# Optimization experiments

Hardware: AMD Instinct MI355X
Metric: run time of the kernel (lower is better)

The kernel has to match this reference:

```python
import jax, jax.numpy as jnp
import numpy as np

N = 100000
IN_CH, HID_CH, OUT_CH = 128, 128, 64
E = 1600000


def gcn_layer(x, W, b, src, dst, num_nodes):
    """PyG GCNConv: add self-loops, symmetric deg^-1/2 normalization,
    x' = D^-1/2 (A+I) D^-1/2 (x W) + b."""
    # degrees including self-loops (deg = 1 + in-degree with unit edge weights)
    ones = jnp.ones(dst.shape[0], dtype=x.dtype)
    deg = jnp.ones(num_nodes, dtype=x.dtype).at[dst].add(ones)
    dinv = jax.lax.rsqrt(deg)
    h = x @ W  # [N, out_dim] -- transform before propagate (PyG order)
    # neighbor messages
    norm = dinv[src] * dinv[dst]                      # [E]
    msg = h[src] * norm[:, None]                      # [E, out_dim] (traffic-bound)
    agg = jax.ops.segment_sum(msg, dst, num_segments=num_nodes)
    # self-loop contribution: norm_ii = dinv[i]^2
    agg = agg + h * (dinv * dinv)[:, None]
    return agg + b


def setup_inputs() -> dict:
    key = jax.random.key(0)
    ks = jax.random.split(key, 7)
    x = jax.random.normal(ks[0], (N, IN_CH), dtype=jnp.float32)
    edge_index = jax.random.randint(ks[1], (2, E), 0, N, dtype=jnp.int64)
    # Glorot-style init like PyG GCNConv
    W1 = jax.random.normal(ks[2], (IN_CH, HID_CH), dtype=jnp.float32) * (1.0 / np.sqrt(IN_CH))
    b1 = jnp.zeros((HID_CH,), dtype=jnp.float32)
    W2 = jax.random.normal(ks[3], (HID_CH, OUT_CH), dtype=jnp.float32) * (1.0 / np.sqrt(HID_CH))
    b2 = jnp.zeros((OUT_CH,), dtype=jnp.float32)
    return {"x": x, "edge_index": edge_index, "W1": W1, "b1": b1, "W2": W2, "b2": b2}


def reference(x, edge_index, W1, b1, W2, b2):
    src, dst = edge_index[0], edge_index[1]
    h = gcn_layer(x, W1, b1, src, dst, N)
    h = jax.nn.relu(h)  # dropout is identity in eval mode
    out = gcn_layer(h, W2, b2, src, dst, N)
    return out
```

## Files before the change

### kernel.cpp

```cpp
#include <hip/hip_runtime.h>
#include <hip/hip_fp16.h>

#define NNODES 100000
#define NEDGES 1600000
#define IN_C   128
#define HID_C  128
#define OUT_C  64

#define CAP     64
#define OVF_MAX 4096

#define BUCKET_SHIFT 7
#define BUCKET_NODES 128
#define NB ((NNODES + BUCKET_NODES - 1) / BUCKET_NODES)
#define BCAP 3072
#define BCNT_STRIDE 16
#define EB 4096
#define NBLK_A ((NEDGES + EB - 1) / EB)
#define GB ((NNODES + 63) / 64)

typedef __attribute__((ext_vector_type(8))) _Float16 half8;
typedef __attribute__((ext_vector_type(4))) _Float16 half4;
typedef __attribute__((ext_vector_type(4))) float floatx4;

__device__ __forceinline__ long long load_idx(const void* p, long long i, int is64) {
  return is64 ? ((const long long*)p)[i] : (long long)((const int*)p)[i];
}

__global__ void prep_kernel(const void* eidx, int* flag, int* bcnt,
                            int* ovf_cnt, int* ovfA_cnt,
                            const float* __restrict__ W1,
                            const float* __restrict__ W2,
                            _Float16* __restrict__ Wt1,
                            _Float16* __restrict__ Wt2) {
  int i = blockIdx.x * 256 + threadIdx.x;
  if (i < NB * BCNT_STRIDE) bcnt[i] = 0;
  if (i == 0) { *ovf_cnt = 0; *ovfA_cnt = 0; }
  if (blockIdx.x == 0 && threadIdx.x < 64) {
    const unsigned* w = (const unsigned*)eidx;
    unsigned v = w[2 * threadIdx.x + 1];
    unsigned long long bad = __ballot(v != 0u);
    if (threadIdx.x == 0) *flag = (bad == 0ull) ? 1 : 0;
  }
  const int stride = gridDim.x * 256;
  for (int t = i; t < IN_C * HID_C; t += stride) {
    int n = t >> 7, k = t & 127;
    Wt1[t] = (_Float16)W1[k * HID_C + n];
  }
  for (int t = i; t < HID_C * OUT_C; t += stride) {
    int n = t >> 7, k = t & 127;
    Wt2[t] = (_Float16)W2[k * OUT_C + n];
  }
}

__global__ __launch_bounds__(512) void binA_kernel(const void* __restrict__ eidx,
                                                   const int* __restrict__ flag,
                                                   int* __restrict__ bcnt,
                                                   unsigned* __restrict__ buf,
                                                   int* __restrict__ ovfA_cnt,
                                                   int2* __restrict__ ovfA) {
  __shared__ unsigned se[EB];
  __shared__ unsigned short be[EB];
  __shared__ int hist[NB];
  __shared__ int base[NB];
  __shared__ int ofs[NB];
  const int tid = threadIdx.x;
  const int e0 = blockIdx.x * EB;
  const int e1 = min(e0 + EB, NEDGES);
  const int m = e1 - e0;
  const int is64 = *flag;

  for (int b = tid; b < NB; b += 512) { hist[b] = 0; ofs[b] = 0; }
  __syncthreads();

  for (int k = tid; k < m; k += 512) {
    int e = e0 + k;
    int s = (int)load_idx(eidx, e, is64);
    int d = (int)load_idx(eidx, (long long)NEDGES + e, is64);
    int b = d >> BUCKET_SHIFT;
    se[k] = (unsigned)s | ((unsigned)(d & (BUCKET_NODES - 1)) << 17);
    be[k] = (unsigned short)b;
    atomicAdd(&hist[b], 1);
  }
  __syncthreads();

  int rot = (blockIdx.x * 131) % NB;
  for (int idx = tid; idx < NB; idx += 512) {
    int b = idx + rot;
    if (b >= NB) b -= NB;
    int h = hist[b];
    if (h > 0) base[b] = atomicAdd(&bcnt[b * BCNT_STRIDE], h);
  }
  __syncthreads();

  for (int k = tid; k < m; k += 512) {
    unsigned u = se[k];
    int b = be[k];
    int ko = atomicAdd(&ofs[b], 1);
    int slot = base[b] + ko;
    if (slot < BCAP) {
      buf[(size_t)b * BCAP + slot] = u;
    } else {
      int p = atomicAdd(ovfA_cnt, 1);
      if (p < OVF_MAX)
        ovfA[p] = make_int2((int)(u & 0x1FFFFu),
                            (b << BUCKET_SHIFT) | (int)(u >> 17));
    }
  }
}

__global__ __launch_bounds__(512) void binB_kernel(const int* __restrict__ bcnt,
                                                   const unsigned* __restrict__ buf,
                                                   const int* __restrict__ ovfA_cnt,
                                                   const int2* __restrict__ ovfA,
                                                   int* __restrict__ cnt,
                                                   float* __restrict__ dinv,
                                                   int* __restrict__ pad_csr,
                                                   int* __restrict__ ovf_cnt,
                                                   int2* __restrict__ ovf) {
  __shared__ int pad[BUCKET_NODES * CAP];
  __shared__ int lcnt[BUCKET_NODES];
  const int b = blockIdx.x;
  const int tid = threadIdx.x;
  const int node0 = b << BUCKET_SHIFT;

  if (tid < BUCKET_NODES) lcnt[tid] = 0;
  __syncthreads();

  const int n = min(bcnt[b * BCNT_STRIDE], BCAP);
  for (int k = tid; k < n; k += 512) {
    unsigned u = buf[(size_t)b * BCAP + k];
    int s = (int)(u & 0x1FFFFu);
    int dl = (int)(u >> 17);
    int slot = atomicAdd(&lcnt[dl], 1);
    if (slot < CAP) {
      pad[dl * CAP + slot] = s;
    } else {
      int p = atomicAdd(ovf_cnt, 1);
      if (p < OVF_MAX) ovf[p] = make_int2(s, node0 + dl);
    }
  }
  int na = min(*ovfA_cnt, OVF_MAX);
  for (int t = tid; t < na; t += 512) {
    int2 p = ovfA[t];
    if ((p.y >> BUCKET_SHIFT) == b) {
      int dl = p.y & (BUCKET_NODES - 1);
      int slot = atomicAdd(&lcnt[dl], 1);
      if (slot < CAP) {
        pad[dl * CAP + slot] = p.x;
      } else {
        int q = atomicAdd(ovf_cnt, 1);
        if (q < OVF_MAX) ovf[q] = make_int2(p.x, p.y);
      }
    }
  }
  __syncthreads();

  constexpr int I4PN = CAP / 4;
  for (int q = tid; q < BUCKET_NODES * I4PN; q += 512) {
    int dl = q / I4PN;
    int gn = node0 + dl;
    if (gn < NNODES) {
      int c = (q % I4PN) * 4;
      *(int4*)&pad_csr[(size_t)gn * CAP + c] = *(const int4*)&pad[dl * CAP + c];
    }
  }
  if (tid < BUCKET_NODES && node0 + tid < NNODES) {
    int c = lcnt[tid];
    cnt[node0 + tid] = c;
    dinv[node0 + tid] = rsqrtf((float)(c + 1));
  }
}

__global__ __launch_bounds__(256) void gemm1_kernel(const float* __restrict__ x,
                                                    const _Float16* __restrict__ Wt1,
                                                    const float* __restrict__ dinv,
                                                    _Float16* __restrict__ h1s) {
  constexpr int K = IN_C, N = HID_C, KP = K + 8;
  __shared__ alignas(16) _Float16 Alds[64 * KP];
  __shared__ alignas(16) _Float16 Wlds[N * KP];
  const int tid = threadIdx.x;
  const int row0 = blockIdx.x * 64;

  for (int idx = tid; idx < N * (K / 8); idx += 256) {
    int n = idx >> 4, k16 = idx & 15;
    *(int4*)&Wlds[n * KP + k16 * 8] = *(const int4*)&Wt1[n * K + k16 * 8];
  }
  constexpr int F4PR = K / 4;
  for (int idx = tid; idx < 64 * F4PR; idx += 256) {
    int lr = idx >> 5;
    int c4 = (idx & 31) * 4;
    int gr = row0 + lr;
    if (gr > NNODES - 1) gr = NNODES - 1;
    float4 v = *(const float4*)&x[(size_t)gr * K + c4];
    half4 h = {(_Float16)v.x, (_Float16)v.y, (_Float16)v.z, (_Float16)v.w};
    *(half4*)&Alds[lr * KP + c4] = h;
  }
  __syncthreads();

  const int w = tid >> 6;
  const int lane = tid & 63;
  const int g = lane >> 4;
  const int mi = lane & 15;
  constexpr int NT = N / 16;
  floatx4 acc[NT];
#pragma unroll
  for (int t = 0; t < NT; ++t) acc[t] = (floatx4){0.f, 0.f, 0.f, 0.f};
  const _Float16* arow = &Alds[(w * 16 + mi) * KP];
#pragma unroll
  for (int ks = 0; ks < K / 32; ++ks) {
    half8 a = *(const half8*)(arow + ks * 32 + g * 8);
#pragma unroll
    for (int t = 0; t < NT; ++t) {
      half8 b = *(const half8*)&Wlds[(t * 16 + mi) * KP + ks * 32 + g * 8];
      acc[t] = __builtin_amdgcn_mfma_f32_16x16x32_f16(a, b, acc[t], 0, 0, 0);
    }
  }
#pragma unroll
  for (int r = 0; r < 4; ++r) {
    int grow = row0 + w * 16 + 4 * g + r;
    if (grow < NNODES) {
      float s = dinv[grow];
      _Float16* orow = h1s + (size_t)grow * N + mi;
#pragma unroll
      for (int t = 0; t < NT; ++t) orow[t * 16] = (_Float16)(acc[t][r] * s);
    }
  }
}

__global__ __launch_bounds__(256) void gemm2_kernel(const _Float16* __restrict__ hid,
                                                    const _Float16* __restrict__ Wt2,
                                                    const float* __restrict__ dinv,
                                                    _Float16* __restrict__ h2s) {
  constexpr int K = HID_C, N = OUT_C, KP = K + 8;
  __shared__ alignas(16) _Float16 Alds[64 * KP];
  __shared__ alignas(16) _Float16 Wlds[N * KP];
  const int tid = threadIdx.x;
  const int row0 = blockIdx.x * 64;

  for (int idx = tid; idx < N * (K / 8); idx += 256) {
    int n = idx >> 4, k16 = idx & 15;
    *(int4*)&Wlds[n * KP + k16 * 8] = *(const int4*)&Wt2[n * K + k16 * 8];
  }
  for (int idx = tid; idx < 64 * (K / 8); idx += 256) {
    int lr = idx >> 4, k16 = idx & 15;
    int gr = row0 + lr;
    if (gr > NNODES - 1) gr = NNODES - 1;
    *(int4*)&Alds[lr * KP + k16 * 8] =
        *(const int4*)&hid[(size_t)gr * K + k16 * 8];
  }
  __syncthreads();

  const int w = tid >> 6;
  const int lane = tid & 63;
  const int g = lane >> 4;
  const int mi = lane & 15;
  constexpr int NT = N / 16;
  floatx4 acc[NT];
#pragma unroll
  for (int t = 0; t < NT; ++t) acc[t] = (floatx4){0.f, 0.f, 0.f, 0.f};
  const _Float16* arow = &Alds[(w * 16 + mi) * KP];
#pragma unroll
  for (int ks = 0; ks < K / 32; ++ks) {
    half8 a = *(const half8*)(arow + ks * 32 + g * 8);
#pragma unroll
    for (int t = 0; t < NT; ++t) {
      half8 b = *(const half8*)&Wlds[(t * 16 + mi) * KP + ks * 32 + g * 8];
      acc[t] = __builtin_amdgcn_mfma_f32_16x16x32_f16(a, b, acc[t], 0, 0, 0);
    }
  }
#pragma unroll
  for (int r = 0; r < 4; ++r) {
    int grow = row0 + w * 16 + 4 * g + r;
    if (grow < NNODES) {
      float s = dinv[grow];
      _Float16* orow = h2s + (size_t)grow * N + mi;
#pragma unroll
      for (int t = 0; t < NT; ++t) orow[t * 16] = (_Float16)(acc[t][r] * s);
    }
  }
}

struct F8 {
  float x0, x1, x2, x3, x4, x5, x6, x7;
};

__device__ __forceinline__ void add_h8(F8& a, const __half* p) {
  int4 r = *(const int4*)p;
  const __half2* h = (const __half2*)&r;
  float2 f0 = __half22float2(h[0]);
  float2 f1 = __half22float2(h[1]);
  float2 f2 = __half22float2(h[2]);
  float2 f3 = __half22float2(h[3]);
  a.x0 += f0.x; a.x1 += f0.y; a.x2 += f1.x; a.x3 += f1.y;
  a.x4 += f2.x; a.x5 += f2.y; a.x6 += f3.x; a.x7 += f3.y;
}

template <int C, bool RELU, bool OUT16>
__global__ __launch_bounds__(256) void gather_kernel(const int* __restrict__ cnt,
                                                     const int* __restrict__ pad_csr,
                                                     const float* __restrict__ dinv,
                                                     const __half* __restrict__ Hs,
                                                     const float* __restrict__ bias,
                                                     const int* __restrict__ ovf_cnt,
                                                     const int2* __restrict__ ovf,
                                                     void* __restrict__ OutPtr) {
  constexpr int TPN = C / 16;
  int gid = blockIdx.x * 256 + threadIdx.x;
  int i = gid / TPN;
  int c16 = (gid % TPN) * 16;
  if (i >= NNODES) return;

  const float di = dinv[i];
  const int deg = cnt[i];
  const int beg = i * CAP;
  const int end = beg + min(deg, CAP);
  const int* __restrict__ lst = pad_csr;
  const __half* __restrict__ Hb = Hs + c16;

  F8 a0l = {}, a0h = {}, a1l = {}, a1h = {};
  {
    const __half* p = Hb + (size_t)i * C;
    add_h8(a0l, p);
    add_h8(a0h, p + 8);
  }

  int j = beg;
  for (; j + 8 <= end; j += 8) {
    int4 sa = *(const int4*)&lst[j];
    int4 sb = *(const int4*)&lst[j + 4];
    const __half* p0 = Hb + (size_t)sa.x * C;
    const __half* p1 = Hb + (size_t)sa.y * C;
    const __half* p2 = Hb + (size_t)sa.z * C;
    const __half* p3 = Hb + (size_t)sa.w * C;
    add_h8(a0l, p0); add_h8(a0h, p0 + 8);
    add_h8(a1l, p1); add_h8(a1h, p1 + 8);
    add_h8(a0l, p2); add_h8(a0h, p2 + 8);
    add_h8(a1l, p3); add_h8(a1h, p3 + 8);
    const __half* p4 = Hb + (size_t)sb.x * C;
    const __half* p5 = Hb + (size_t)sb.y * C;
    const __half* p6 = Hb + (size_t)sb.z * C;
    const __half* p7 = Hb + (size_t)sb.w * C;
    add_h8(a0l, p4); add_h8(a0h, p4 + 8);
    add_h8(a1l, p5); add_h8(a1h, p5 + 8);
    add_h8(a0l, p6); add_h8(a0h, p6 + 8);
    add_h8(a1l, p7); add_h8(a1h, p7 + 8);
  }
  for (; j + 2 <= end; j += 2) {
    const __half* p0 = Hb + (size_t)lst[j] * C;
    const __half* p1 = Hb + (size_t)lst[j + 1] * C;
    add_h8(a0l, p0); add_h8(a0h, p0 + 8);
    add_h8(a1l, p1); add_h8(a1h, p1 + 8);
  }
  if (j < end) {
    const __half* p0 = Hb + (size_t)lst[j] * C;
    add_h8(a0l, p0); add_h8(a0h, p0 + 8);
  }

  if (deg > CAP) {
    int n = min(*ovf_cnt, OVF_MAX);
    for (int t = 0; t < n; ++t) {
      int2 p = ovf[t];
      if (p.y == i) {
        const __half* q = Hb + (size_t)p.x * C;
        add_h8(a0l, q); add_h8(a0h, q + 8);
      }
    }
  }

  float s0 = a0l.x0 + a1l.x0, s1 = a0l.x1 + a1l.x1;
  float s2 = a0l.x2 + a1l.x2, s3 = a0l.x3 + a1l.x3;
  float s4 = a0l.x4 + a1l.x4, s5 = a0l.x5 + a1l.x5;
  float s6 = a0l.x6 + a1l.x6, s7 = a0l.x7 + a1l.x7;
  float s8 = a0h.x0 + a1h.x0, s9 = a0h.x1 + a1h.x1;
  float s10 = a0h.x2 + a1h.x2, s11 = a0h.x3 + a1h.x3;
  float s12 = a0h.x4 + a1h.x4, s13 = a0h.x5 + a1h.x5;
  float s14 = a0h.x6 + a1h.x6, s15 = a0h.x7 + a1h.x7;

  float4 b0 = *(const float4*)&bias[c16];
  float4 b1 = *(const float4*)&bias[c16 + 4];
  float4 b2 = *(const float4*)&bias[c16 + 8];
  float4 b3 = *(const float4*)&bias[c16 + 12];
  float o0 = fmaf(s0, di, b0.x),  o1 = fmaf(s1, di, b0.y);
  float o2 = fmaf(s2, di, b0.z),  o3 = fmaf(s3, di, b0.w);
  float o4 = fmaf(s4, di, b1.x),  o5 = fmaf(s5, di, b1.y);
  float o6 = fmaf(s6, di, b1.z),  o7 = fmaf(s7, di, b1.w);
  float o8 = fmaf(s8, di, b2.x),  o9 = fmaf(s9, di, b2.y);
  float o10 = fmaf(s10, di, b2.z), o11 = fmaf(s11, di, b2.w);
  float o12 = fmaf(s12, di, b3.x), o13 = fmaf(s13, di, b3.y);
  float o14 = fmaf(s14, di, b3.z), o15 = fmaf(s15, di, b3.w);
  if (RELU) {
    o0 = o0 > 0.f ? o0 : 0.f;   o1 = o1 > 0.f ? o1 : 0.f;
    o2 = o2 > 0.f ? o2 : 0.f;   o3 = o3 > 0.f ? o3 : 0.f;
    o4 = o4 > 0.f ? o4 : 0.f;   o5 = o5 > 0.f ? o5 : 0.f;
    o6 = o6 > 0.f ? o6 : 0.f;   o7 = o7 > 0.f ? o7 : 0.f;
    o8 = o8 > 0.f ? o8 : 0.f;   o9 = o9 > 0.f ? o9 : 0.f;
    o10 = o10 > 0.f ? o10 : 0.f; o11 = o11 > 0.f ? o11 : 0.f;
    o12 = o12 > 0.f ? o12 : 0.f; o13 = o13 > 0.f ? o13 : 0.f;
    o14 = o14 > 0.f ? o14 : 0.f; o15 = o15 > 0.f ? o15 : 0.f;
  }
  if (OUT16) {
    _Float16* Out = (_Float16*)OutPtr + (size_t)i * C + c16;
    half8 hv0 = {(_Float16)o0, (_Float16)o1, (_Float16)o2, (_Float16)o3,
                 (_Float16)o4, (_Float16)o5, (_Float16)o6, (_Float16)o7};
    half8 hv1 = {(_Float16)o8, (_Float16)o9, (_Float16)o10, (_Float16)o11,
                 (_Float16)o12, (_Float16)o13, (_Float16)o14, (_Float16)o15};
    *(half8*)Out = hv0;
    *(half8*)(Out + 8) = hv1;
  } else {
    float* Out = (float*)OutPtr + (size_t)i * C + c16;
    *(float4*)Out = make_float4(o0, o1, o2, o3);
    *(float4*)(Out + 4) = make_float4(o4, o5, o6, o7);
    *(float4*)(Out + 8) = make_float4(o8, o9, o10, o11);
    *(float4*)(Out + 12) = make_float4(o12, o13, o14, o15);
  }
}

extern "C" void kernel_launch(void* const* d_in, const int* in_sizes, int n_in,
                              void* d_out, int out_size, void* d_ws, size_t ws_size,
                              hipStream_t stream) {
  const float* x = (const float*)d_in[0];
  const void* eidx = d_in[1];
  const float* W1 = (const float*)d_in[2];
  const float* b1 = (const float*)d_in[3];
  const float* W2 = (const float*)d_in[4];
  const float* b2 = (const float*)d_in[5];
  float* out = (float*)d_out;
  char* ws = (char*)d_ws;

  int*      flag     = (int*)(ws + 0);
  int*      ovf_cnt  = (int*)(ws + 512);
  int*      ovfA_cnt = (int*)(ws + 1024);
  int*      bcnt     = (int*)(ws + 1536);
  int*      cnt      = (int*)(ws + 52224);
  float*    dinv     = (float*)(ws + 452608);
  int2*     ovf      = (int2*)(ws + 852992);
  int2*     ovfA     = (int2*)(ws + 885760);
  _Float16* Wt1      = (_Float16*)(ws + 918528);
  _Float16* Wt2      = (_Float16*)(ws + 951296);
  unsigned* buf      = (unsigned*)(ws + 968192);
  int*      pad_csr  = (int*)(ws + 10577920);
  _Float16* h1s      = (_Float16*)(ws + 36178432);
  _Float16* hidden   = (_Float16*)(ws + 61778944);
  _Float16* h2s      = h1s;

  prep_kernel<<<(NB * BCNT_STRIDE + 255) / 256, 256, 0, stream>>>(
      eidx, flag, bcnt, ovf_cnt, ovfA_cnt, W1, W2, Wt1, Wt2);
  binA_kernel<<<NBLK_A, 512, 0, stream>>>(eidx, flag, bcnt, buf, ovfA_cnt, ovfA);
  binB_kernel<<<NB, 512, 0, stream>>>(bcnt, buf, ovfA_cnt, ovfA, cnt, dinv,
                                      pad_csr, ovf_cnt, ovf);
  gemm1_kernel<<<GB, 256, 0, stream>>>(x, Wt1, dinv, h1s);
  gather_kernel<HID_C, true, true>
      <<<(NNODES * (HID_C / 16) + 255) / 256, 256, 0, stream>>>(
          cnt, pad_csr, dinv, (const __half*)h1s, b1, ovf_cnt, ovf, hidden);
  gemm2_kernel<<<GB, 256, 0, stream>>>(hidden, Wt2, dinv, h2s);
  gather_kernel<OUT_C, false, false>
      <<<(NNODES * (OUT_C / 16) + 255) / 256, 256, 0, stream>>>(
          cnt, pad_csr, dinv, (const __half*)h2s, b2, ovf_cnt, ovf, out);
}
```

Measured before the change: 270.4 us.

## Fuse graph-build kernels into one cooperative kernel and halve padded CSR capacity

Merges the prep, bin-A and bin-B kernels into a single cooperative kernel that uses grid-wide syncs between phases, removing two kernel launches and their gaps. It also reduces the per-node padded neighbour capacity from 64 to 32, which halves pad_csr writes and gather index reads. The catch is that more nodes exceed the capacity and go to the overflow path, where the overflow list is capped at 4096 entries. Cooperative launch also requires all 391 blocks of 512 threads to be co-resident.

```diff
diff --git a/kernel.cpp b/kernel.cpp
--- a/kernel.cpp
+++ b/kernel.cpp
@@ -1,5 +1,8 @@
 #include <hip/hip_runtime.h>
 #include <hip/hip_fp16.h>
+#include <hip/hip_cooperative_groups.h>
+
+namespace cg = cooperative_groups;
 
 #define NNODES 100000
 #define NEDGES 1600000
@@ -7,7 +10,7 @@
 #define HID_C  128
 #define OUT_C  64
 
-#define CAP     64
+#define CAP     32
 #define OVF_MAX 4096
 
 #define BUCKET_SHIFT 7
@@ -27,148 +30,142 @@
   return is64 ? ((const long long*)p)[i] : (long long)((const int*)p)[i];
 }
 
-__global__ void prep_kernel(const void* eidx, int* flag, int* bcnt,
-                            int* ovf_cnt, int* ovfA_cnt,
-                            const float* __restrict__ W1,
-                            const float* __restrict__ W2,
-                            _Float16* __restrict__ Wt1,
-                            _Float16* __restrict__ Wt2) {
-  int i = blockIdx.x * 256 + threadIdx.x;
-  if (i < NB * BCNT_STRIDE) bcnt[i] = 0;
-  if (i == 0) { *ovf_cnt = 0; *ovfA_cnt = 0; }
-  if (blockIdx.x == 0 && threadIdx.x < 64) {
+__global__ __launch_bounds__(512, 4) void build_kernel(
+    const void* __restrict__ eidx, int* __restrict__ flag,
+    int* __restrict__ bcnt, unsigned* __restrict__ buf,
+    int* __restrict__ ovfA_cnt, int2* __restrict__ ovfA,
+    int* __restrict__ cnt, float* __restrict__ dinv,
+    int* __restrict__ pad_csr, int* __restrict__ ovf_cnt,
+    int2* __restrict__ ovf,
+    const float* __restrict__ W1, const float* __restrict__ W2,
+    _Float16* __restrict__ Wt1, _Float16* __restrict__ Wt2) {
+  __shared__ alignas(16) char smem[34304];
+  const int tid = threadIdx.x;
+  const int gid = blockIdx.x * 512 + tid;
+  cg::grid_group grid = cg::this_grid();
+
+  for (int i = gid; i < NB * BCNT_STRIDE; i += NBLK_A * 512) bcnt[i] = 0;
+  if (gid == 0) { *ovf_cnt = 0; *ovfA_cnt = 0; }
+  if (blockIdx.x == 0 && tid < 64) {
     const unsigned* w = (const unsigned*)eidx;
-    unsigned v = w[2 * threadIdx.x + 1];
+    unsigned v = w[2 * tid + 1];
     unsigned long long bad = __ballot(v != 0u);
-    if (threadIdx.x == 0) *flag = (bad == 0ull) ? 1 : 0;
-  }
-  const int stride = gridDim.x * 256;
-  for (int t = i; t < IN_C * HID_C; t += stride) {
+    if (tid == 0) *flag = (bad == 0ull) ? 1 : 0;
+  }
+  for (int t = gid; t < IN_C * HID_C; t += NBLK_A * 512) {
     int n = t >> 7, k = t & 127;
     Wt1[t] = (_Float16)W1[k * HID_C + n];
   }
-  for (int t = i; t < HID_C * OUT_C; t += stride) {
+  for (int t = gid; t < HID_C * OUT_C; t += NBLK_A * 512) {
     int n = t >> 7, k = t & 127;
     Wt2[t] = (_Float16)W2[k * OUT_C + n];
   }
-}
-
-__global__ __launch_bounds__(512) void binA_kernel(const void* __restrict__ eidx,
-                                                   const int* __restrict__ flag,
-                                                   int* __restrict__ bcnt,
-                                                   unsigned* __restrict__ buf,
-                                                   int* __restrict__ ovfA_cnt,
-                                                   int2* __restrict__ ovfA) {
-  __shared__ unsigned se[EB];
-  __shared__ unsigned short be[EB];
-  __shared__ int hist[NB];
-  __shared__ int base[NB];
-  __shared__ int ofs[NB];
-  const int tid = threadIdx.x;
-  const int e0 = blockIdx.x * EB;
-  const int e1 = min(e0 + EB, NEDGES);
-  const int m = e1 - e0;
-  const int is64 = *flag;
-
-  for (int b = tid; b < NB; b += 512) { hist[b] = 0; ofs[b] = 0; }
-  __syncthreads();
-
-  for (int k = tid; k < m; k += 512) {
-    int e = e0 + k;
-    int s = (int)load_idx(eidx, e, is64);
-    int d = (int)load_idx(eidx, (long long)NEDGES + e, is64);
-    int b = d >> BUCKET_SHIFT;
-    se[k] = (unsigned)s | ((unsigned)(d & (BUCKET_NODES - 1)) << 17);
-    be[k] = (unsigned short)b;
-    atomicAdd(&hist[b], 1);
-  }
-  __syncthreads();
-
-  int rot = (blockIdx.x * 131) % NB;
-  for (int idx = tid; idx < NB; idx += 512) {
-    int b = idx + rot;
-    if (b >= NB) b -= NB;
-    int h = hist[b];
-    if (h > 0) base[b] = atomicAdd(&bcnt[b * BCNT_STRIDE], h);
-  }
-  __syncthreads();
-
-  for (int k = tid; k < m; k += 512) {
-    unsigned u = se[k];
-    int b = be[k];
-    int ko = atomicAdd(&ofs[b], 1);
-    int slot = base[b] + ko;
-    if (slot < BCAP) {
-      buf[(size_t)b * BCAP + slot] = u;
-    } else {
-      int p = atomicAdd(ovfA_cnt, 1);
-      if (p < OVF_MAX)
-        ovfA[p] = make_int2((int)(u & 0x1FFFFu),
-                            (b << BUCKET_SHIFT) | (int)(u >> 17));
-    }
-  }
-}
-
-__global__ __launch_bounds__(512) void binB_kernel(const int* __restrict__ bcnt,
-                                                   const unsigned* __restrict__ buf,
-                                                   const int* __restrict__ ovfA_cnt,
-                                                   const int2* __restrict__ ovfA,
-                                                   int* __restrict__ cnt,
-                                                   float* __restrict__ dinv,
-                                                   int* __restrict__ pad_csr,
-                                                   int* __restrict__ ovf_cnt,
-                                                   int2* __restrict__ ovf) {
-  __shared__ int pad[BUCKET_NODES * CAP];
-  __shared__ int lcnt[BUCKET_NODES];
-  const int b = blockIdx.x;
-  const int tid = threadIdx.x;
-  const int node0 = b << BUCKET_SHIFT;
-
-  if (tid < BUCKET_NODES) lcnt[tid] = 0;
-  __syncthreads();
-
-  const int n = min(bcnt[b * BCNT_STRIDE], BCAP);
-  for (int k = tid; k < n; k += 512) {
-    unsigned u = buf[(size_t)b * BCAP + k];
-    int s = (int)(u & 0x1FFFFu);
-    int dl = (int)(u >> 17);
-    int slot = atomicAdd(&lcnt[dl], 1);
-    if (slot < CAP) {
-      pad[dl * CAP + slot] = s;
-    } else {
-      int p = atomicAdd(ovf_cnt, 1);
-      if (p < OVF_MAX) ovf[p] = make_int2(s, node0 + dl);
-    }
-  }
-  int na = min(*ovfA_cnt, OVF_MAX);
-  for (int t = tid; t < na; t += 512) {
-    int2 p = ovfA[t];
-    if ((p.y >> BUCKET_SHIFT) == b) {
-      int dl = p.y & (BUCKET_NODES - 1);
-      int slot = atomicAdd(&lcnt[dl], 1);
-      if (slot < CAP) {
-        pad[dl * CAP + slot] = p.x;
+  grid.sync();
+
+  {
+    unsigned* se = (unsigned*)smem;
+    unsigned short* be = (unsigned short*)(smem + 16384);
+    int* hist = (int*)(smem + 24576);
+    int* base = (int*)(smem + 27712);
+    int* ofs  = (int*)(smem + 30848);
+    const int e0 = blockIdx.x * EB;
+    const int e1 = min(e0 + EB, NEDGES);
+    const int m = e1 - e0;
+    const int is64 = *flag;
+
+    for (int b = tid; b < NB; b += 512) { hist[b] = 0; ofs[b] = 0; }
+    __syncthreads();
+
+    for (int k = tid; k < m; k += 512) {
+      int e = e0 + k;
+      int s = (int)load_idx(eidx, e, is64);
+      int d = (int)load_idx(eidx, (long long)NEDGES + e, is64);
+      int b = d >> BUCKET_SHIFT;
+      se[k] = (unsigned)s | ((unsigned)(d & (BUCKET_NODES - 1)) << 17);
+      be[k] = (unsigned short)b;
+      atomicAdd(&hist[b], 1);
+    }
+    __syncthreads();
+
+    int rot = (blockIdx.x * 131) % NB;
+    for (int idx = tid; idx < NB; idx += 512) {
+      int b = idx + rot;
+      if (b >= NB) b -= NB;
+      int h = hist[b];
+      if (h > 0) base[b] = atomicAdd(&bcnt[b * BCNT_STRIDE], h);
+    }
+    __syncthreads();
+
+    for (int k = tid; k < m; k += 512) {
+      unsigned u = se[k];
+      int b = be[k];
+      int ko = atomicAdd(&ofs[b], 1);
+      int slot = base[b] + ko;
+      if (slot < BCAP) {
+        buf[(size_t)b * BCAP + slot] = u;
       } else {
-        int q = atomicAdd(ovf_cnt, 1);
-        if (q < OVF_MAX) ovf[q] = make_int2(p.x, p.y);
-      }
-    }
-  }
-  __syncthreads();
-
-  constexpr int I4PN = CAP / 4;
-  for (int q = tid; q < BUCKET_NODES * I4PN; q += 512) {
-    int dl = q / I4PN;
-    int gn = node0 + dl;
-    if (gn < NNODES) {
-      int c = (q % I4PN) * 4;
-      *(int4*)&pad_csr[(size_t)gn * CAP + c] = *(const int4*)&pad[dl * CAP + c];
-    }
-  }
-  if (tid < BUCKET_NODES && node0 + tid < NNODES) {
-    int c = lcnt[tid];
-    cnt[node0 + tid] = c;
-    dinv[node0 + tid] = rsqrtf((float)(c + 1));
+        int p = atomicAdd(ovfA_cnt, 1);
+        if (p < OVF_MAX)
+          ovfA[p] = make_int2((int)(u & 0x1FFFFu),
+                              (b << BUCKET_SHIFT) | (int)(u >> 17));
+      }
+    }
+  }
+  grid.sync();
+
+  {
+    int* pad = (int*)smem;
+    int* lcnt = (int*)(smem + 16384);
+    for (int b = blockIdx.x; b < NB; b += NBLK_A) {
+      const int node0 = b << BUCKET_SHIFT;
+      if (tid < BUCKET_NODES) lcnt[tid] = 0;
+      __syncthreads();
+
+      const int n = min(bcnt[b * BCNT_STRIDE], BCAP);
+      for (int k = tid; k < n; k += 512) {
+        unsigned u = buf[(size_t)b * BCAP + k];
+        int s = (int)(u & 0x1FFFFu);
+        int dl = (int)(u >> 17);
+        int slot = atomicAdd(&lcnt[dl], 1);
+        if (slot < CAP) {
+          pad[dl * CAP + slot] = s;
+        } else {
+          int p = atomicAdd(ovf_cnt, 1);
+          if (p < OVF_MAX) ovf[p] = make_int2(s, node0 + dl);
+        }
+      }
+      int na = min(*ovfA_cnt, OVF_MAX);
+      for (int t = tid; t < na; t += 512) {
+        int2 p = ovfA[t];
+        if ((p.y >> BUCKET_SHIFT) == b) {
+          int dl = p.y & (BUCKET_NODES - 1);
+          int slot = atomicAdd(&lcnt[dl], 1);
+          if (slot < CAP) {
+            pad[dl * CAP + slot] = p.x;
+          } else {
+            int q = atomicAdd(ovf_cnt, 1);
+            if (q < OVF_MAX) ovf[q] = make_int2(p.x, p.y);
+          }
+        }
+      }
+      __syncthreads();
+
+      constexpr int I4PN = CAP / 4;
+      for (int q = tid; q < BUCKET_NODES * I4PN; q += 512) {
+        int dl = q / I4PN;
+        int gn = node0 + dl;
+        if (gn < NNODES) {
+          int c = (q % I4PN) * 4;
+          *(int4*)&pad_csr[(size_t)gn * CAP + c] = *(const int4*)&pad[dl * CAP + c];
+        }
+      }
+      if (tid < BUCKET_NODES && node0 + tid < NNODES) {
+        int c = lcnt[tid];
+        cnt[node0 + tid] = c;
+        dinv[node0 + tid] = rsqrtf((float)(c + 1));
+      }
+      __syncthreads();
+    }
   }
 }
 
@@ -440,15 +437,18 @@
   _Float16* Wt2      = (_Float16*)(ws + 951296);
   unsigned* buf      = (unsigned*)(ws + 968192);
   int*      pad_csr  = (int*)(ws + 10577920);
-  _Float16* h1s      = (_Float16*)(ws + 36178432);
-  _Float16* hidden   = (_Float16*)(ws + 61778944);
+  _Float16* h1s      = (_Float16*)(ws + 23378432);
+  _Float16* hidden   = (_Float16*)(ws + 48978944);
   _Float16* h2s      = h1s;
 
-  prep_kernel<<<(NB * BCNT_STRIDE + 255) / 256, 256, 0, stream>>>(
-      eidx, flag, bcnt, ovf_cnt, ovfA_cnt, W1, W2, Wt1, Wt2);
-  binA_kernel<<<NBLK_A, 512, 0, stream>>>(eidx, flag, bcnt, buf, ovfA_cnt, ovfA);
-  binB_kernel<<<NB, 512, 0, stream>>>(bcnt, buf, ovfA_cnt, ovfA, cnt, dinv,
-                                      pad_csr, ovf_cnt, ovf);
+  {
+    void* args[] = {(void*)&eidx, (void*)&flag, (void*)&bcnt, (void*)&buf,
+                    (void*)&ovfA_cnt, (void*)&ovfA, (void*)&cnt, (void*)&dinv,
+                    (void*)&pad_csr, (void*)&ovf_cnt, (void*)&ovf,
+                    (void*)&W1, (void*)&W2, (void*)&Wt1, (void*)&Wt2};
+    hipLaunchCooperativeKernel((const void*)build_kernel, dim3(NBLK_A), dim3(512),
+                               args, 0, stream);
+  }
   gemm1_kernel<<<GB, 256, 0, stream>>>(x, Wt1, dinv, h1s);
   gather_kernel<HID_C, true, true>
       <<<(NNODES * (HID_C / 16) + 255) / 256, 256, 0, stream>>>(
```

Result: slower. 384.3 us (+42.1%).
